# Optimization experiments

Hardware: AMD Instinct MI355X
Metric: run time of the kernel (lower is better)

The kernel has to match this reference:

```python
import jax, jax.numpy as jnp
import numpy as np

NUM_R = 725
NUM_T = 180
EPS = 1e-6


def _hough(img):
    """Discrete Hough transform: params[r, t] = sum of img along line
    x*cos(theta_t) + y*sin(theta_t) = rho_r.
    Gather form: sweep along the longer axis of the line (x-sweep when
    |sin|>=|cos|, else y-sweep) so every line is sampled densely.
    """
    W, H = img.shape  # assume square (W == H) so both sweeps share length
    diag = jnp.sqrt(jnp.asarray(W * W + H * H, dtype=img.dtype))
    thetas = jnp.arange(NUM_T, dtype=img.dtype) * (jnp.pi / NUM_T)      # [T]
    rhos = jnp.linspace(-diag, diag, NUM_R, dtype=img.dtype)            # [R]
    cos_t = jnp.cos(thetas)                                             # [T]
    sin_t = jnp.sin(thetas)                                             # [T]
    n = jnp.arange(W)                                                   # sweep coord [N]
    nf = n.astype(img.dtype)

    rho_b = rhos[:, None, None]          # [R,1,1]
    cos_b = cos_t[None, :, None]         # [1,T,1]
    sin_b = sin_t[None, :, None]
    n_b = nf[None, None, :]              # [1,1,N]

    # --- x-sweep: x = n, y = (rho - x*cos) / sin ---
    sin_safe = jnp.where(jnp.abs(sin_b) < EPS, jnp.asarray(1.0, img.dtype), sin_b)
    y_f = (rho_b - n_b * cos_b) / sin_safe
    y_i = jnp.round(y_f).astype(jnp.int32)                              # [R,T,N]
    valid_x = (y_i >= 0) & (y_i < H)
    vals_x = jnp.where(valid_x,
                       img[n[None, None, :], jnp.clip(y_i, 0, H - 1)],
                       jnp.asarray(0.0, img.dtype))

    # --- y-sweep: y = n, x = (rho - y*sin) / cos ---
    cos_safe = jnp.where(jnp.abs(cos_b) < EPS, jnp.asarray(1.0, img.dtype), cos_b)
    x_f = (rho_b - n_b * sin_b) / cos_safe
    x_i = jnp.round(x_f).astype(jnp.int32)
    valid_y = (x_i >= 0) & (x_i < W)
    vals_y = jnp.where(valid_y,
                       img[jnp.clip(x_i, 0, W - 1), n[None, None, :]],
                       jnp.asarray(0.0, img.dtype))

    use_x = (jnp.abs(sin_t) >= jnp.abs(cos_t))[None, :, None]           # [1,T,1]
    vals = jnp.where(use_x, vals_x, vals_y)
    return jnp.sum(vals, axis=-1)                                        # [R,T]


def setup_inputs() -> dict:
    key = jax.random.key(0)
    img = jax.random.uniform(key, (512, 512), dtype=jnp.float32)
    return {"img": img}


def reference(img):
    return _hough(img)
```

## Files before the change

### kernel.cpp

```cpp
#include <hip/hip_runtime.h>
#include <math.h>

#define W 512
#define H 512
#define NUM_R 725
#define NUM_T 180
#define RCHUNK 32
#define NCHUNK (H / RCHUNK)
#define RPAD 768

#define WS_FLOATS ((size_t)W * H + (size_t)NCHUNK * NUM_T * RPAD)

__global__ __launch_bounds__(256) void transpose_k(const float* __restrict__ in,
                                                   float* __restrict__ out) {
    __shared__ float tile[32][33];
    const int bx = blockIdx.x * 32, by = blockIdx.y * 32;
    const int tx = threadIdx.x, ty = threadIdx.y;
#pragma unroll
    for (int j = 0; j < 32; j += 8)
        tile[ty + j][tx] = in[(size_t)(by + ty + j) * W + (bx + tx)];
    __syncthreads();
#pragma unroll
    for (int j = 0; j < 32; j += 8)
        out[(size_t)(bx + ty + j) * H + (by + tx)] = tile[tx][ty + j];
}

__global__ __launch_bounds__(256) void hough_scatter_k(const float* __restrict__ img,
                                                       const float* __restrict__ imgT,
                                                       float* __restrict__ partial) {
    const int t   = blockIdx.x;
    const int n0  = blockIdx.y * RCHUNK;
    const int tid = threadIdx.x;
    const int wave = tid >> 6;

    __shared__ float racc[4 * RPAD];

    {
        float4* z = (float4*)racc;
#pragma unroll
        for (int k = 0; k < 3; ++k)
            z[tid + 256 * k] = make_float4(0.f, 0.f, 0.f, 0.f);
    }
    __syncthreads();

    const double theta = (double)t * (M_PI / 180.0);
    const double s = sin(theta);
    const double c = cos(theta);
    const bool use_x = fabs(s) >= fabs(c);
    const double diag = sqrt(524288.0);
    const double step = (2.0 * diag) / 724.0;
    const double inv_step = 1.0 / step;

    const double lane_co = (use_x ? s : c) * inv_step;
    const double loop_co = (use_x ? c : s) * inv_step;
    const double dstep   = diag * inv_step;

    const double SC = 4294967296.0;
    const long long laneq = (long long)rint(lane_co * SC);
    const long long lq    = (long long)rint(loop_co * SC);
    const long long lq2   = 2 * lq;
    const long long L1 = laneq, L2 = 2 * laneq, L3 = 3 * laneq;
    const unsigned hwq = (unsigned)(fabs(lane_co) * 0.5 * SC);
    const unsigned B = 2u * hwq;

    const int h  = tid >> 7;
    const int c0 = (tid & 127) * 4;
    const double rowpart = (double)(n0 + h) * loop_co + dstep;
    long long u = (long long)rint((rowpart + (double)c0 * lane_co) * SC)
                + (long long)hwq;

    float* racc_w = racc + wave * RPAD;
    const float* __restrict__ base = use_x ? img : imgT;
    const float4* rowp = (const float4*)(base + (size_t)(n0 + h) * W) + (tid & 127);

#pragma unroll
    for (int j = 0; j < RCHUNK / 2; ++j) {
        const float4 v = rowp[j * (2 * W / 4)];
        const long long u0 = u;
        const long long u1 = u + L1;
        const long long u2 = u + L2;
        const long long u3 = u + L3;
        u += lq2;
        const float a0 = ((unsigned)u0 <= B) ? v.x : 0.f;
        const float a1 = ((unsigned)u1 <= B) ? v.y : 0.f;
        const float a2 = ((unsigned)u2 <= B) ? v.z : 0.f;
        const float a3 = ((unsigned)u3 <= B) ? v.w : 0.f;
        racc_w[(int)(u0 >> 32)] += a0;
        racc_w[(int)(u1 >> 32)] += a1;
        racc_w[(int)(u2 >> 32)] += a2;
        racc_w[(int)(u3 >> 32)] += a3;
    }

    __syncthreads();

    float* dst = partial + ((size_t)blockIdx.y * NUM_T + t) * RPAD;
#pragma unroll
    for (int k = 0; k < 3; ++k) {
        const int r = tid + 256 * k;
        dst[r] = racc[r] + racc[RPAD + r] + racc[2 * RPAD + r] + racc[3 * RPAD + r];
    }
}

__global__ __launch_bounds__(256) void reduce_k(const float* __restrict__ partial,
                                                float* __restrict__ out) {
    const int t = blockIdx.x;
    const int tid = threadIdx.x;
#pragma unroll
    for (int k = 0; k < 3; ++k) {
        const int r = tid + 256 * k;
        if (r < NUM_R) {
            float acc = 0.f;
#pragma unroll
            for (int ch = 0; ch < NCHUNK; ++ch)
                acc += partial[((size_t)ch * NUM_T + t) * RPAD + r];
            out[(size_t)r * NUM_T + t] = acc;
        }
    }
}

__global__ __launch_bounds__(256) void hough_gather_k(const float* __restrict__ img,
                                                      float* __restrict__ out) {
    const int t = blockIdx.x;
    const int r = blockIdx.y * 256 + threadIdx.x;
    const int rc = (r < NUM_R) ? r : (NUM_R - 1);

    const double theta = (double)t * (M_PI / 180.0);
    const double s = sin(theta);
    const double c = cos(theta);
    const bool use_x = fabs(s) >= fabs(c);
    double dd = use_x ? s : c;
    if (fabs(dd) < 1e-6) dd = 1.0;
    const double a = use_x ? c : s;
    const double inv = 1.0 / dd;
    const double nk2 = -(a * inv);
    const double diag = sqrt(524288.0);
    const double step = (2.0 * diag) / 724.0;
    double rho = (double)rc * step - diag;
    if (rc == NUM_R - 1) rho = diag;

    const double SCALE = 1099511627776.0;
    const long long NK2q = (long long)rint(nk2 * SCALE);
    long long Y = (long long)rint(rho * inv * SCALE) + (1ll << 39);

    float acc = 0.f;
    if (use_x) {
#pragma unroll 8
        for (int n = 0; n < W; ++n) {
            const int y = (int)(Y >> 40);
            Y += NK2q;
            const float v = img[n * W + min(max(y, 0), W - 1)];
            acc += ((unsigned)y < (unsigned)W) ? v : 0.f;
        }
    } else {
#pragma unroll 4
        for (int n = 0; n < W; ++n) {
            const int y = (int)(Y >> 40);
            Y += NK2q;
            const float v = img[min(max(y, 0), W - 1) * W + n];
            acc += ((unsigned)y < (unsigned)W) ? v : 0.f;
        }
    }
    if (r < NUM_R) out[(size_t)r * NUM_T + t] = acc;
}

extern "C" void kernel_launch(void* const* d_in, const int* in_sizes, int n_in,
                              void* d_out, int out_size, void* d_ws, size_t ws_size,
                              hipStream_t stream) {
    const float* img = (const float*)d_in[0];
    float* out = (float*)d_out;

    if (ws_size >= WS_FLOATS * sizeof(float)) {
        float* imgT    = (float*)d_ws;
        float* partial = (float*)d_ws + (size_t)W * H;

        transpose_k<<<dim3(16, 16), dim3(32, 8), 0, stream>>>(img, imgT);
        hough_scatter_k<<<dim3(NUM_T, NCHUNK), dim3(256), 0, stream>>>(img, imgT, partial);
        reduce_k<<<dim3(NUM_T), dim3(256), 0, stream>>>(partial, out);
    } else {
        hough_gather_k<<<dim3(NUM_T, (NUM_R + 255) / 256), dim3(256), 0, stream>>>(img, out);
    }
}
```

Baseline: 76.33 us.

## Batch register accumulation across rows before scattering into LDS histogram

```diff
diff --git a/kernel.cpp b/kernel.cpp
--- a/kernel.cpp
+++ b/kernel.cpp
@@ -25,6 +25,33 @@
         out[(size_t)(bx + ty + j) * H + (by + tx)] = tile[tx][ty + j];
 }
 
+template <int P>
+__device__ __forceinline__ void run16(const float4* __restrict__ rp, int rstep,
+                                      long long u, long long lqa,
+                                      long long L1, long long L2, long long L3,
+                                      unsigned B, float* __restrict__ racc_w) {
+#pragma unroll
+    for (int per = 0; per < 16 / P; ++per) {
+        float a0 = 0.f, a1 = 0.f, a2 = 0.f, a3 = 0.f;
+        long long u0 = 0, u1 = 0, u2 = 0, u3 = 0;
+#pragma unroll
+        for (int p = 0; p < P; ++p) {
+            const float4 v = rp[(per * P + p) * rstep];
+            u0 = u; u1 = u + L1; u2 = u + L2; u3 = u + L3;
+            a0 += ((unsigned)u0 <= B) ? v.x : 0.f;
+            a1 += ((unsigned)u1 <= B) ? v.y : 0.f;
+            a2 += ((unsigned)u2 <= B) ? v.z : 0.f;
+            a3 += ((unsigned)u3 <= B) ? v.w : 0.f;
+            if (p < P - 1) u += lqa;
+        }
+        racc_w[(int)(u0 >> 32)] += a0;
+        racc_w[(int)(u1 >> 32)] += a1;
+        racc_w[(int)(u2 >> 32)] += a2;
+        racc_w[(int)(u3 >> 32)] += a3;
+        u += lqa;
+    }
+}
+
 __global__ __launch_bounds__(256) void hough_scatter_k(const float* __restrict__ img,
                                                        const float* __restrict__ imgT,
                                                        float* __restrict__ partial) {
@@ -54,41 +81,41 @@
     const double lane_co = (use_x ? s : c) * inv_step;
     const double loop_co = (use_x ? c : s) * inv_step;
     const double dstep   = diag * inv_step;
+    const double lane_a  = fabs(lane_co);
+    const double loop_a  = fabs(loop_co);
 
     const double SC = 4294967296.0;
     const long long laneq = (long long)rint(lane_co * SC);
-    const long long lq    = (long long)rint(loop_co * SC);
-    const long long lq2   = 2 * lq;
+    const long long lqa   = llabs((long long)rint(loop_co * SC));
     const long long L1 = laneq, L2 = 2 * laneq, L3 = 3 * laneq;
-    const unsigned hwq = (unsigned)(fabs(lane_co) * 0.5 * SC);
+    const unsigned hwq = (unsigned)(lane_a * 0.5 * SC);
     const unsigned B = 2u * hwq;
+
+    int P = 2;
+    if      (lane_a + 15.0 * loop_a < 0.98) P = 16;
+    else if (lane_a +  7.0 * loop_a < 0.98) P = 8;
+    else if (lane_a +  3.0 * loop_a < 0.98) P = 4;
 
     const int h  = tid >> 7;
     const int c0 = (tid & 127) * 4;
-    const double rowpart = (double)(n0 + h) * loop_co + dstep;
-    long long u = (long long)rint((rowpart + (double)c0 * lane_co) * SC)
+    const int rbase = n0 + 16 * h;
+    const bool neg = (loop_co < 0.0);
+    const int rstart = neg ? rbase + 15 : rbase;
+    const int rstep  = neg ? -(W / 4) : (W / 4);
+
+    long long u = (long long)rint(((double)rstart * loop_co +
+                                   (double)c0 * lane_co + dstep) * SC)
                 + (long long)hwq;
 
     float* racc_w = racc + wave * RPAD;
     const float* __restrict__ base = use_x ? img : imgT;
-    const float4* rowp = (const float4*)(base + (size_t)(n0 + h) * W) + (tid & 127);
-
-#pragma unroll
-    for (int j = 0; j < RCHUNK / 2; ++j) {
-        const float4 v = rowp[j * (2 * W / 4)];
-        const long long u0 = u;
-        const long long u1 = u + L1;
-        const long long u2 = u + L2;
-        const long long u3 = u + L3;
-        u += lq2;
-        const float a0 = ((unsigned)u0 <= B) ? v.x : 0.f;
-        const float a1 = ((unsigned)u1 <= B) ? v.y : 0.f;
-        const float a2 = ((unsigned)u2 <= B) ? v.z : 0.f;
-        const float a3 = ((unsigned)u3 <= B) ? v.w : 0.f;
-        racc_w[(int)(u0 >> 32)] += a0;
-        racc_w[(int)(u1 >> 32)] += a1;
-        racc_w[(int)(u2 >> 32)] += a2;
-        racc_w[(int)(u3 >> 32)] += a3;
+    const float4* rp = (const float4*)base + (size_t)rstart * (W / 4) + (tid & 127);
+
+    switch (P) {
+        case 16: run16<16>(rp, rstep, u, lqa, L1, L2, L3, B, racc_w); break;
+        case 8:  run16<8> (rp, rstep, u, lqa, L1, L2, L3, B, racc_w); break;
+        case 4:  run16<4> (rp, rstep, u, lqa, L1, L2, L3, B, racc_w); break;
+        default: run16<2> (rp, rstep, u, lqa, L1, L2, L3, B, racc_w); break;
     }
 
     __syncthreads();
```

After: 73.02 us. 4.3% less time.
